# Kernel tuning notes

Measured on AMD Instinct MI355X. Metric: run time of the kernel, lower is better.

The kernel has to match this reference:

```python
import jax, jax.numpy as jnp
import numpy as np

MAX_PER_CLASS = 100   # max_num_boxes_per_class
MAX_TOTAL = 300       # max_num_boxes (pad_per_class=False -> output size is MAX_TOTAL)
IOU_THR = 0.5
SCORE_THR = 0.001
NEG = jnp.float32(-1e30)
EPS = 1e-12


def _canon(b):
    # boxes given as any diagonal pair (y1,x1,y2,x2); canonicalize like TF NMS
    ymin = jnp.minimum(b[..., 0], b[..., 2])
    ymax = jnp.maximum(b[..., 0], b[..., 2])
    xmin = jnp.minimum(b[..., 1], b[..., 3])
    xmax = jnp.maximum(b[..., 1], b[..., 3])
    return ymin, xmin, ymax, xmax


def _iou_one_vs_all(box, boxes):
    # box [4], boxes [N,4] -> iou [N]
    y1a, x1a, y2a, x2a = _canon(box)
    y1b, x1b, y2b, x2b = _canon(boxes)
    ih = jnp.maximum(jnp.minimum(y2a, y2b) - jnp.maximum(y1a, y1b), 0.0)
    iw = jnp.maximum(jnp.minimum(x2a, x2b) - jnp.maximum(x1a, x1b), 0.0)
    inter = ih * iw
    area_a = (y2a - y1a) * (x2a - x1a)
    area_b = (y2b - y1b) * (x2b - x1b)
    union = jnp.maximum(area_a + area_b - inter, EPS)
    return inter / union


def _nms_single_class(boxes_c, scores_c):
    # boxes_c [N,4], scores_c [N] -> (scores [K], boxes [K,4], valid [K]) with K=MAX_PER_CLASS
    N = scores_c.shape[0]
    valid = scores_c > SCORE_THR
    s = jnp.where(valid, scores_c, NEG)
    order = jnp.argsort(-s)
    b_sorted = boxes_c[order]          # [N,4]
    s_sorted = s[order]                # [N]
    v_sorted = valid[order]            # [N]

    def step(keep, xs):
        i, box_i, valid_i = xs
        iou_row = _iou_one_vs_all(box_i, b_sorted)          # [N]
        suppressed = jnp.any(keep & (iou_row > IOU_THR))    # vs previously kept only
        keep = keep.at[i].set(valid_i & jnp.logical_not(suppressed))
        return keep, None

    keep0 = jnp.zeros((N,), dtype=bool)
    keep, _ = jax.lax.scan(step, keep0, (jnp.arange(N), b_sorted, v_sorted))

    # cap number of kept boxes at MAX_PER_CLASS (in descending score order)
    rank = jnp.cumsum(keep.astype(jnp.int32)) - 1
    keep = keep & (rank < MAX_PER_CLASS)

    key = jnp.where(keep, s_sorted, NEG)
    top_s, top_i = jax.lax.top_k(key, MAX_PER_CLASS)
    top_boxes = b_sorted[top_i]
    top_valid = top_s > (NEG / 2)
    return top_s, top_boxes, top_valid


def _combined_nms(scores, boxes):
    # scores [B,N,C], boxes [B,N,q,4] with q==1 (boxes shared across classes)
    B, N, C = scores.shape
    q = boxes.shape[2]

    def per_image(scores_i, boxes_i):
        # scores_i [N,C], boxes_i [N,q,4]
        if q == 1:
            cls_boxes = jnp.broadcast_to(boxes_i, (N, C, 4))
        else:
            cls_boxes = boxes_i
        # per-class NMS, vmapped over the class axis
        sc, bx, vd = jax.vmap(_nms_single_class, in_axes=(1, 1))(cls_boxes, scores_i)
        # sc [C,K], bx [C,K,4], vd [C,K]
        cls_ids = jnp.broadcast_to(
            jnp.arange(C, dtype=scores.dtype)[:, None], vd.shape)

        flat_s = jnp.where(vd, sc, NEG).reshape(-1)   # [C*K]
        flat_b = bx.reshape(-1, 4)
        flat_c = cls_ids.reshape(-1)
        flat_v = vd.reshape(-1)

        top_s, idx = jax.lax.top_k(flat_s, MAX_TOTAL)
        out_v = flat_v[idx]
        out_s = jnp.where(out_v, top_s, 0.0)
        out_b = jnp.where(out_v[:, None], flat_b[idx], 0.0)
        out_b = jnp.clip(out_b, 0.0, 1.0)             # clip_boxes=True
        out_c = jnp.where(out_v, flat_c[idx], 0.0)
        count = jnp.sum(out_v.astype(jnp.int32))
        return out_s, out_b, out_c, count

    return jax.vmap(per_image)(scores, boxes)


def setup_inputs() -> dict:
    key = jax.random.key(0)
    k1, k2 = jax.random.split(key)
    B, N, C, Q = 4, 1024, 80, 1
    scores = jax.random.uniform(k1, (B, N, C), dtype=jnp.float32)
    boxes = jax.random.uniform(k2, (B, N, Q, 4), dtype=jnp.float32)
    return {"scores": scores, "boxes": boxes}


def reference(scores, boxes):
    # returns (output_scores, output_boxes, output_classes, valid_counts)
    return _combined_nms(scores, boxes)
```

## Files before the change

### kernel.cpp

```cpp
#include <hip/hip_runtime.h>
#include <stdint.h>

#define N_BOX 1024
#define C_CLS 80
#define B_IMG 4
#define K_PER 100
#define K_TOT 300
#define NEGF  (-1e30f)
#define NCAND (C_CLS * K_PER)
#define M_SEL 8192
#define KPAD  1088
#define EQCAP 768

#define OFF_DONE    0
#define OFF_WSCORE  1835008
#define OFF_WSIDX   1963008

typedef unsigned long long u64;
typedef unsigned int u32;

__device__ __forceinline__ int swz(int i) { return i + (i >> 4); }

__device__ __forceinline__ u32 ford(float f) {
    u32 u = __float_as_uint(f);
    return (u & 0x80000000u) ? ~u : (u | 0x80000000u);
}
__device__ __forceinline__ float funord(u32 o) {
    u32 u = (o & 0x80000000u) ? (o ^ 0x80000000u) : ~o;
    return __uint_as_float(u);
}

__device__ __forceinline__ bool iou_gt_fast(float4 a, float aa, float4 b, float ab) {
#pragma clang fp contract(off)
    float ih = fminf(a.z, b.z) - fmaxf(a.x, b.x); ih = fmaxf(ih, 0.0f);
    float iw = fminf(a.w, b.w) - fmaxf(a.y, b.y); iw = fmaxf(iw, 0.0f);
    float inter = ih * iw;
    float uni = fmaxf(aa + ab - inter, 1e-12f);
    float diff = 2.0f * inter - uni;
    bool kill = diff > uni * 2.4e-7f;
    if (__builtin_expect(!kill && diff > 0.0f, 0))
        kill = (inter / uni) > 0.5f;
    return kill;
}

__global__ __launch_bounds__(256, 2) void nms_classes(
        const float* __restrict__ scores,
        const float* __restrict__ boxes,
        float* __restrict__ ws_score,
        int*   __restrict__ ws_idx,
        float* __restrict__ out,
        int*   __restrict__ done_cnt)
{
    __shared__ u64    key[KPAD];
    __shared__ float4 bx[N_BOX];
    __shared__ float  ar[N_BOX];
    __shared__ float4 wbuf[2][64];
    __shared__ float  wab[2][64];
    __shared__ float4 kb[128];
    __shared__ float  ka[128];
    __shared__ int    kept_t[K_PER];
    __shared__ u32    colk16[4][64];
    __shared__ u64    sup64[4];
    __shared__ int    sh_nvalid, sh_kept, sh_rank;
    __shared__ u32    skey[NCAND];
    __shared__ u32    hist4[1024];
    __shared__ u64    list[512];
    __shared__ u32    eq[EQCAP];
    __shared__ int    sh_sel, sh_cnt, sh_valid, sh_eqcnt;
    __shared__ u32    sh_need;

    const int tid  = threadIdx.x;
    const int lane = tid & 63;
    const int b  = blockIdx.x / C_CLS;
    const int c  = blockIdx.x % C_CLS;

    if (tid == 0) { sh_nvalid = 0; sh_kept = 0; }

    for (int n = tid; n < N_BOX; n += 256) {
        float4 v = ((const float4*)boxes)[b * N_BOX + n];
        {
#pragma clang fp contract(off)
            float y1 = fminf(v.x, v.z), y2 = fmaxf(v.x, v.z);
            float x1 = fminf(v.y, v.w), x2 = fmaxf(v.y, v.w);
            bx[n] = make_float4(y1, x1, y2, x2);
            ar[n] = (y2 - y1) * (x2 - x1);
        }
    }
    __syncthreads();

    u64 r[4];
    {
        const float* sc = scores + (size_t)(b * N_BOX) * C_CLS + c;
        int lv = 0;
        #pragma unroll
        for (int q = 0; q < 4; ++q) {
            int v = tid * 4 + q;
            float s0 = sc[(size_t)v * C_CLS];
            bool valid = s0 > 0.001f;
            float s = valid ? s0 : NEGF;
            r[q] = ((u64)ford(s) << 32) | (u32)(N_BOX - 1 - v);
            lv += valid ? 1 : 0;
        }
        if (lv) atomicAdd(&sh_nvalid, lv);
    }

    #define CE(a, b, d) { u64 _mx = (a) > (b) ? (a) : (b); \
                          u64 _mn = (a) > (b) ? (b) : (a); \
                          (a) = (d) ? _mx : _mn; (b) = (d) ? _mn : _mx; }
    CE(r[0], r[1], true); CE(r[2], r[3], false);

    for (int k = 4; k <= N_BOX; k <<= 1) {
        const bool d = ((tid & (k >> 2)) == 0);
        for (int j = k >> 1; j > 0; j >>= 1) {
            if (j >= 256) {
                __syncthreads();
                #pragma unroll
                for (int q = 0; q < 4; ++q) key[swz(tid * 4 + q)] = r[q];
                __syncthreads();
                const bool upper = ((tid * 4) & j) != 0;
                #pragma unroll
                for (int q = 0; q < 4; ++q) {
                    u64 pv = key[swz((tid * 4 + q) ^ j)];
                    u64 mx = r[q] > pv ? r[q] : pv;
                    u64 mn = r[q] > pv ? pv : r[q];
                    r[q] = (d != upper) ? mx : mn;
                }
            } else if (j >= 4) {
                const int dl = j >> 2;
                const bool upper = (lane & dl) != 0;
                #pragma unroll
                for (int q = 0; q < 4; ++q) {
                    u64 pv = __shfl_xor(r[q], dl);
                    u64 mx = r[q] > pv ? r[q] : pv;
                    u64 mn = r[q] > pv ? pv : r[q];
                    r[q] = (d != upper) ? mx : mn;
                }
            } else if (j == 2) {
                CE(r[0], r[2], d); CE(r[1], r[3], d);
            } else {
                CE(r[0], r[1], d); CE(r[2], r[3], d);
            }
        }
    }
    #undef CE

    __syncthreads();
    #pragma unroll
    for (int q = 0; q < 4; ++q) key[swz(tid * 4 + q)] = r[q];
    __syncthreads();

    if (tid < 64) {
        u64 kv = key[swz(tid)];
        int idx = (N_BOX - 1) - (int)(u32)(kv & 0xFFFFFFFFu);
        wbuf[0][tid] = bx[idx];
        wab[0][tid]  = ar[idx];
    }

    const int nvalid = sh_nvalid;
    const int nwin = (nvalid + 63) >> 6;
    const int me  = tid & 63;
    const int grp = tid >> 6;

    for (int w = 0; w < nwin; ++w) {
        const int cur = w & 1;
        __syncthreads();
        if (sh_kept >= K_PER) break;
        const int kept0 = sh_kept;
        const int bt = w * 64;

        if (grp == 1 && (w + 1) < nwin) {
            u64 kv = key[swz((bt + 64 + me) & (N_BOX - 1))];
            int idx = (N_BOX - 1) - (int)(u32)(kv & 0xFFFFFFFFu);
            wbuf[cur ^ 1][me] = bx[idx];
            wab[cur ^ 1][me]  = ar[idx];
        }

        const float4 qm = wbuf[cur][me];
        const float  am = wab[cur][me];

        {
            float4 wrow[16]; float warow[16];
            #pragma unroll
            for (int rq = 0; rq < 16; ++rq) {
                wrow[rq]  = wbuf[cur][grp * 16 + rq];
                warow[rq] = wab[cur][grp * 16 + rq];
            }
            u32 bits = 0;
            #pragma unroll
            for (int rq = 0; rq < 16; ++rq) {
                int rr = grp * 16 + rq;
                bool kill = (rr != me) && iou_gt_fast(wrow[rq], warow[rq], qm, am);
                bits |= ((u32)kill) << rq;
            }
            colk16[grp][me] = bits;
        }

        {
            bool supme = false;
            for (int t0 = 0; grp + 4 * t0 < kept0; t0 += 8) {
                float4 kbl[8]; float kal[8];
                #pragma unroll
                for (int i = 0; i < 8; ++i) {
                    int k = grp + 4 * (t0 + i);
                    kbl[i] = kb[k]; kal[i] = ka[k];
                }
                #pragma unroll
                for (int i = 0; i < 8; ++i) {
                    int k = grp + 4 * (t0 + i);
                    if (k < kept0 && iou_gt_fast(kbl[i], kal[i], qm, am)) supme = true;
                }
            }
            u64 bal = __ballot(supme);
            if (lane == 0) sup64[grp] = bal;
        }
        __syncthreads();

        if (grp == 0) {
            u32 c0 = colk16[0][lane], c1 = colk16[1][lane];
            u32 c2 = colk16[2][lane], c3 = colk16[3][lane];
            u64 colkill = (u64)c0 | ((u64)c1 << 16)
                        | ((u64)c2 << 32) | ((u64)c3 << 48);
            u64 supp = sup64[0] | sup64[1] | sup64[2] | sup64[3];
            bool in = ((bt + lane) < nvalid) && !((supp >> lane) & 1ull);
            u64 pending = __ballot(in);
            int kept = kept0;
            u64 acc = 0;
            while (pending && kept < K_PER) {
                int t0 = __ffsll((long long)pending) - 1;
                acc |= 1ull << t0;
                kept++;
                bool kill = (colkill >> t0) & 1ull;
                pending &= ~(1ull << t0);
                pending &= ~__ballot(kill);
            }
            if ((acc >> lane) & 1ull) {
                int pos = kept0 + (int)__popcll(acc & ((1ull << lane) - 1ull));
                kept_t[pos] = bt + lane;
                kb[pos] = qm; ka[pos] = am;
            }
            if (lane == 0) sh_kept = kept;
        }
    }
    __syncthreads();

    const int kept = sh_kept;
    if (tid < K_PER) {
        int ob = (b * C_CLS + c) * K_PER + tid;
        if (tid < kept) {
            u64 k = key[swz(kept_t[tid])];
            ws_score[ob] = funord((u32)(k >> 32));
            ws_idx[ob]   = (N_BOX - 1) - (int)(u32)(k & 0xFFFFFFFFu);
        } else {
            ws_score[ob] = NEGF;
            ws_idx[ob]   = 0;
        }
    }

    __syncthreads();
    if (tid == 0) {
        __threadfence();
        sh_rank = atomicAdd(&done_cnt[b], 1);
    }
    __syncthreads();
    if (sh_rank != C_CLS - 1) return;
    __threadfence();

    const int base2 = b * NCAND;
    if (tid == 0) { sh_cnt = 0; sh_valid = 0; sh_eqcnt = 0; }
    for (int i = tid; i < NCAND / 4; i += 256) {
        float4 s4 = ((const float4*)(ws_score + base2))[i];
        skey[4 * i + 0] = ford(s4.x);
        skey[4 * i + 1] = ford(s4.y);
        skey[4 * i + 2] = ford(s4.z);
        skey[4 * i + 3] = ford(s4.w);
    }
    for (int i = tid; i < 512; i += 256) list[i] = 0;
    for (int i = tid; i < 1024; i += 256) hist4[i] = 0;
    __syncthreads();

    u64 prefix = 0;
    u32 need = K_TOT;
    const int rounds[6] = {7, 6, 5, 4, 1, 0};
    const int slot = tid & 3;

    for (int rd = 0; rd < 2; ++rd) {
        const int d = rounds[rd];
        for (int i0 = 0; i0 < NCAND; i0 += 1024) {
            u32 kv[4];
            #pragma unroll
            for (int q = 0; q < 4; ++q) {
                int i = i0 + tid + q * 256;
                kv[q] = (i < NCAND) ? skey[i] : 0u;
            }
            #pragma unroll
            for (int q = 0; q < 4; ++q) {
                int i = i0 + tid + q * 256;
                if (i < NCAND) {
                    u64 k = ((u64)kv[q] << 32) | (u32)(M_SEL - 1 - i);
                    bool match = (d == 7) || (((k ^ prefix) >> (8 * (d + 1))) == 0);
                    if (match)
                        atomicAdd(&hist4[(((u32)(k >> (8 * d)) & 0xFFu) << 2) | slot], 1u);
                }
            }
        }
        __syncthreads();
        if (tid < 64) {
            const int l = tid;
            u32 h[4];
            #pragma unroll
            for (int q = 0; q < 4; ++q) {
                int bin = 4 * l + q;
                h[q] = hist4[bin * 4 + 0] + hist4[bin * 4 + 1]
                     + hist4[bin * 4 + 2] + hist4[bin * 4 + 3];
                hist4[bin * 4 + 0] = 0; hist4[bin * 4 + 1] = 0;
                hist4[bin * 4 + 2] = 0; hist4[bin * 4 + 3] = 0;
            }
            u32 s3 = h[3], s2 = h[2] + s3, s1 = h[1] + s2, s0 = h[0] + s1;
            u32 tot = s0, S = tot;
            #pragma unroll
            for (int off = 1; off < 64; off <<= 1) {
                u32 t = __shfl(S, (l + off) & 63);
                if (l + off < 64) S += t;
            }
            u32 T = S - tot;
            u32 sv0 = s0 + T, sv1 = s1 + T, sv2 = s2 + T, sv3 = s3 + T;
            if (sv0 >= need && sv1 < need) { sh_sel = 4*l;     sh_need = need - sv1; }
            if (sv1 >= need && sv2 < need) { sh_sel = 4*l + 1; sh_need = need - sv2; }
            if (sv2 >= need && sv3 < need) { sh_sel = 4*l + 2; sh_need = need - sv3; }
            if (sv3 >= need && T   < need) { sh_sel = 4*l + 3; sh_need = need - T;   }
        }
        __syncthreads();
        prefix |= ((u64)(u32)sh_sel) << (8 * d);
        need = sh_need;
        __syncthreads();
    }

    {
        const u32 p16 = (u32)(prefix >> 48);
        for (int i0 = 0; i0 < NCAND; i0 += 1024) {
            u32 kv[4];
            #pragma unroll
            for (int q = 0; q < 4; ++q) {
                int i = i0 + tid + q * 256;
                kv[q] = (i < NCAND) ? skey[i] : 0u;
            }
            #pragma unroll
            for (int q = 0; q < 4; ++q) {
                int i = i0 + tid + q * 256;
                if (i < NCAND) {
                    u64 k = ((u64)kv[q] << 32) | (u32)(M_SEL - 1 - i);
                    u32 t16 = (u32)(k >> 48);
                    if (t16 > p16) {
                        int p = atomicAdd(&sh_cnt, 1);
                        if (p < 512) list[p] = k;
                    } else if (t16 == p16) {
                        int p = atomicAdd(&sh_eqcnt, 1);
                        if (p < EQCAP) eq[p] = (u32)i;
                    }
                }
            }
        }
    }
    __syncthreads();
    const int eqn_raw = sh_eqcnt;
    const bool over = eqn_raw > EQCAP;
    const int eqn = over ? 0 : eqn_raw;

    if (!over) {
        for (int rd = 2; rd < 6; ++rd) {
            const int d = rounds[rd];
            for (int j = tid; j < eqn; j += 256) {
                int i = eq[j];
                u64 k = ((u64)skey[i] << 32) | (u32)(M_SEL - 1 - i);
                bool match = (((k ^ prefix) >> (8 * (d + 1))) == 0);
                if (match)
                    atomicAdd(&hist4[(((u32)(k >> (8 * d)) & 0xFFu) << 2) | slot], 1u);
            }
            __syncthreads();
            if (tid < 64) {
                const int l = tid;
                u32 h[4];
                #pragma unroll
                for (int q = 0; q < 4; ++q) {
                    int bin = 4 * l + q;
                    h[q] = hist4[bin * 4 + 0] + hist4[bin * 4 + 1]
                         + hist4[bin * 4 + 2] + hist4[bin * 4 + 3];
                    hist4[bin * 4 + 0] = 0; hist4[bin * 4 + 1] = 0;
                    hist4[bin * 4 + 2] = 0; hist4[bin * 4 + 3] = 0;
                }
                u32 s3 = h[3], s2 = h[2] + s3, s1 = h[1] + s2, s0 = h[0] + s1;
                u32 tot = s0, S = tot;
                #pragma unroll
                for (int off = 1; off < 64; off <<= 1) {
                    u32 t = __shfl(S, (l + off) & 63);
                    if (l + off < 64) S += t;
                }
                u32 T = S - tot;
                u32 sv0 = s0 + T, sv1 = s1 + T, sv2 = s2 + T, sv3 = s3 + T;
                if (sv0 >= need && sv1 < need) { sh_sel = 4*l;     sh_need = need - sv1; }
                if (sv1 >= need && sv2 < need) { sh_sel = 4*l + 1; sh_need = need - sv2; }
                if (sv2 >= need && sv3 < need) { sh_sel = 4*l + 2; sh_need = need - sv3; }
                if (sv3 >= need && T   < need) { sh_sel = 4*l + 3; sh_need = need - T;   }
            }
            __syncthreads();
            prefix |= ((u64)(u32)sh_sel) << (8 * d);
            need = sh_need;
            __syncthreads();
        }

        for (int j = tid; j < eqn; j += 256) {
            int i = eq[j];
            u64 k = ((u64)skey[i] << 32) | (u32)(M_SEL - 1 - i);
            if (k >= prefix) {
                int p = atomicAdd(&sh_cnt, 1);
                if (p < 512) list[p] = k;
            }
        }
    } else {
        __syncthreads();
        for (int i = tid; i < 512; i += 256) list[i] = 0;
        if (tid == 0) sh_cnt = 0;
        __syncthreads();
        for (int rd = 2; rd < 6; ++rd) {
            const int d = rounds[rd];
            for (int i0 = 0; i0 < NCAND; i0 += 1024) {
                u32 kv[4];
                #pragma unroll
                for (int q = 0; q < 4; ++q) {
                    int i = i0 + tid + q * 256;
                    kv[q] = (i < NCAND) ? skey[i] : 0u;
                }
                #pragma unroll
                for (int q = 0; q < 4; ++q) {
                    int i = i0 + tid + q * 256;
                    if (i < NCAND) {
                        u64 k = ((u64)kv[q] << 32) | (u32)(M_SEL - 1 - i);
                        bool match = (((k ^ prefix) >> (8 * (d + 1))) == 0);
                        if (match)
                            atomicAdd(&hist4[(((u32)(k >> (8 * d)) & 0xFFu) << 2) | slot], 1u);
                    }
                }
            }
            __syncthreads();
            if (tid < 64) {
                const int l = tid;
                u32 h[4];
                #pragma unroll
                for (int q = 0; q < 4; ++q) {
                    int bin = 4 * l + q;
                    h[q] = hist4[bin * 4 + 0] + hist4[bin * 4 + 1]
                         + hist4[bin * 4 + 2] + hist4[bin * 4 + 3];
                    hist4[bin * 4 + 0] = 0; hist4[bin * 4 + 1] = 0;
                    hist4[bin * 4 + 2] = 0; hist4[bin * 4 + 3] = 0;
                }
                u32 s3 = h[3], s2 = h[2] + s3, s1 = h[1] + s2, s0 = h[0] + s1;
                u32 tot = s0, S = tot;
                #pragma unroll
                for (int off = 1; off < 64; off <<= 1) {
                    u32 t = __shfl(S, (l + off) & 63);
                    if (l + off < 64) S += t;
                }
                u32 T = S - tot;
                u32 sv0 = s0 + T, sv1 = s1 + T, sv2 = s2 + T, sv3 = s3 + T;
                if (sv0 >= need && sv1 < need) { sh_sel = 4*l;     sh_need = need - sv1; }
                if (sv1 >= need && sv2 < need) { sh_sel = 4*l + 1; sh_need = need - sv2; }
                if (sv2 >= need && sv3 < need) { sh_sel = 4*l + 2; sh_need = need - sv3; }
                if (sv3 >= need && T   < need) { sh_sel = 4*l + 3; sh_need = need - T;   }
            }
            __syncthreads();
            prefix |= ((u64)(u32)sh_sel) << (8 * d);
            need = sh_need;
            __syncthreads();
        }
        for (int i0 = 0; i0 < NCAND; i0 += 1024) {
            u32 kv[4];
            #pragma unroll
            for (int q = 0; q < 4; ++q) {
                int i = i0 + tid + q * 256;
                kv[q] = (i < NCAND) ? skey[i] : 0u;
            }
            #pragma unroll
            for (int q = 0; q < 4; ++q) {
                int i = i0 + tid + q * 256;
                if (i < NCAND) {
                    u64 k = ((u64)kv[q] << 32) | (u32)(M_SEL - 1 - i);
                    if (k >= prefix) {
                        int p = atomicAdd(&sh_cnt, 1);
                        if (p < 512) list[p] = k;
                    }
                }
            }
        }
    }
    __syncthreads();

    if (tid < 64) {
        const int l = tid;
        u64 e[8];
        #pragma unroll
        for (int q = 0; q < 8; ++q) e[q] = list[l * 8 + q];
        #define CE2(a, b, dd) { u64 _mx = (a) > (b) ? (a) : (b); \
                                u64 _mn = (a) > (b) ? (b) : (a); \
                                (a) = (dd) ? _mx : _mn; (b) = (dd) ? _mn : _mx; }
        CE2(e[0], e[1], true);  CE2(e[2], e[3], false);
        CE2(e[4], e[5], true);  CE2(e[6], e[7], false);
        CE2(e[0], e[2], true);  CE2(e[1], e[3], true);
        CE2(e[4], e[6], false); CE2(e[5], e[7], false);
        CE2(e[0], e[1], true);  CE2(e[2], e[3], true);
        CE2(e[4], e[5], false); CE2(e[6], e[7], false);
        for (int k = 8; k <= 512; k <<= 1) {
            const bool d = ((l & (k >> 3)) == 0);
            for (int j = k >> 1; j >= 8; j >>= 1) {
                const int dl = j >> 3;
                const bool upper = (l & dl) != 0;
                #pragma unroll
                for (int q = 0; q < 8; ++q) {
                    u64 pv = __shfl_xor(e[q], dl);
                    u64 mx = e[q] > pv ? e[q] : pv;
                    u64 mn = e[q] > pv ? pv : e[q];
                    e[q] = (d != upper) ? mx : mn;
                }
            }
            CE2(e[0], e[4], d); CE2(e[1], e[5], d);
            CE2(e[2], e[6], d); CE2(e[3], e[7], d);
            CE2(e[0], e[2], d); CE2(e[1], e[3], d);
            CE2(e[4], e[6], d); CE2(e[5], e[7], d);
            CE2(e[0], e[1], d); CE2(e[2], e[3], d);
            CE2(e[4], e[5], d); CE2(e[6], e[7], d);
        }
        #undef CE2
        #pragma unroll
        for (int q = 0; q < 8; ++q) list[l * 8 + q] = e[q];
    }
    __syncthreads();

    float* out_s = out;
    float* out_b = out + B_IMG * K_TOT;
    float* out_c = out + B_IMG * K_TOT * 5;
    float* out_n = out + B_IMG * K_TOT * 6;

    for (int i = tid; i < K_TOT; i += 256) {
        u64 k = list[i];
        float s = funord((u32)(k >> 32));
        int flat = (M_SEL - 1) - (int)(u32)(k & 0xFFFFFFFFu);
        bool valid = s > (-5e29f);
        float os = 0.0f, oc = 0.0f;
        float4 obv = make_float4(0.0f, 0.0f, 0.0f, 0.0f);
        if (valid && flat < NCAND) {
            int cc = flat / K_PER;
            int n  = ws_idx[base2 + flat];
            float4 bb = ((const float4*)boxes)[b * N_BOX + n];
            os = s;
            oc = (float)cc;
            obv.x = fminf(fmaxf(bb.x, 0.0f), 1.0f);
            obv.y = fminf(fmaxf(bb.y, 0.0f), 1.0f);
            obv.z = fminf(fmaxf(bb.z, 0.0f), 1.0f);
            obv.w = fminf(fmaxf(bb.w, 0.0f), 1.0f);
            atomicAdd(&sh_valid, 1);
        }
        out_s[b * K_TOT + i] = os;
        ((float4*)out_b)[b * K_TOT + i] = obv;
        out_c[b * K_TOT + i] = oc;
    }
    __syncthreads();
    if (tid == 0) out_n[b] = (float)sh_valid;
}

extern "C" void kernel_launch(void* const* d_in, const int* in_sizes, int n_in,
                              void* d_out, int out_size, void* d_ws, size_t ws_size,
                              hipStream_t stream) {
    const float* scores = (const float*)d_in[0];
    const float* boxes  = (const float*)d_in[1];

    char* ws = (char*)d_ws;
    int*   done_cnt = (int*)(ws + OFF_DONE);
    float* ws_score = (float*)(ws + OFF_WSCORE);
    int*   ws_idx   = (int*)  (ws + OFF_WSIDX);

    hipMemsetAsync(done_cnt, 0, B_IMG * sizeof(int), stream);
    nms_classes<<<dim3(B_IMG * C_CLS), dim3(256), 0, stream>>>(
        scores, boxes, ws_score, ws_idx, (float*)d_out, done_cnt);
}
```

Measured before the change: 120.1 us.

## Split final cross-class top-k into separate 1024-thread kernel

Removes the last-block-done pattern (memset of counters, threadfence, atomic rank) from the per-class NMS kernel and moves the per-image top-300 radix select into a second kernel launched with one 1024-thread block per image. This drops the large merge-stage shared arrays from the NMS kernel, shrinking its LDS footprint, and lets the final select run with four times as many threads. In exchange it adds a kernel launch boundary and a global round-trip of the workspace between kernels.

```diff
diff --git a/kernel.cpp b/kernel.cpp
--- a/kernel.cpp
+++ b/kernel.cpp
@@ -12,7 +12,6 @@
 #define KPAD  1088
 #define EQCAP 768
 
-#define OFF_DONE    0
 #define OFF_WSCORE  1835008
 #define OFF_WSIDX   1963008
 
@@ -47,9 +46,7 @@
         const float* __restrict__ scores,
         const float* __restrict__ boxes,
         float* __restrict__ ws_score,
-        int*   __restrict__ ws_idx,
-        float* __restrict__ out,
-        int*   __restrict__ done_cnt)
+        int*   __restrict__ ws_idx)
 {
     __shared__ u64    key[KPAD];
     __shared__ float4 bx[N_BOX];
@@ -61,13 +58,7 @@
     __shared__ int    kept_t[K_PER];
     __shared__ u32    colk16[4][64];
     __shared__ u64    sup64[4];
-    __shared__ int    sh_nvalid, sh_kept, sh_rank;
-    __shared__ u32    skey[NCAND];
-    __shared__ u32    hist4[1024];
-    __shared__ u64    list[512];
-    __shared__ u32    eq[EQCAP];
-    __shared__ int    sh_sel, sh_cnt, sh_valid, sh_eqcnt;
-    __shared__ u32    sh_need;
+    __shared__ int    sh_nvalid, sh_kept;
 
     const int tid  = threadIdx.x;
     const int lane = tid & 63;
@@ -255,27 +246,35 @@
             ws_idx[ob]   = 0;
         }
     }
-
-    __syncthreads();
-    if (tid == 0) {
-        __threadfence();
-        sh_rank = atomicAdd(&done_cnt[b], 1);
-    }
-    __syncthreads();
-    if (sh_rank != C_CLS - 1) return;
-    __threadfence();
-
-    const int base2 = b * NCAND;
+}
+
+__global__ __launch_bounds__(1024) void final_topk(
+        const float* __restrict__ ws_score,
+        const int*   __restrict__ ws_idx,
+        const float* __restrict__ boxes,
+        float* __restrict__ out)
+{
+    __shared__ u32 skey[NCAND];
+    __shared__ u32 hist4[1024];
+    __shared__ u64 list[512];
+    __shared__ u32 eq[EQCAP];
+    __shared__ int sh_sel, sh_cnt, sh_valid, sh_eqcnt;
+    __shared__ u32 sh_need;
+
+    const int tid = threadIdx.x;
+    const int b = blockIdx.x;
+    const int base = b * NCAND;
+
     if (tid == 0) { sh_cnt = 0; sh_valid = 0; sh_eqcnt = 0; }
-    for (int i = tid; i < NCAND / 4; i += 256) {
-        float4 s4 = ((const float4*)(ws_score + base2))[i];
+    for (int i = tid; i < NCAND / 4; i += 1024) {
+        float4 s4 = ((const float4*)(ws_score + base))[i];
         skey[4 * i + 0] = ford(s4.x);
         skey[4 * i + 1] = ford(s4.y);
         skey[4 * i + 2] = ford(s4.z);
         skey[4 * i + 3] = ford(s4.w);
     }
-    for (int i = tid; i < 512; i += 256) list[i] = 0;
-    for (int i = tid; i < 1024; i += 256) hist4[i] = 0;
+    if (tid < 512) list[tid] = 0;
+    hist4[tid] = 0;
     __syncthreads();
 
     u64 prefix = 0;
@@ -285,16 +284,16 @@
 
     for (int rd = 0; rd < 2; ++rd) {
         const int d = rounds[rd];
-        for (int i0 = 0; i0 < NCAND; i0 += 1024) {
+        for (int i0 = 0; i0 < NCAND; i0 += 4096) {
             u32 kv[4];
             #pragma unroll
             for (int q = 0; q < 4; ++q) {
-                int i = i0 + tid + q * 256;
+                int i = i0 + tid + q * 1024;
                 kv[q] = (i < NCAND) ? skey[i] : 0u;
             }
             #pragma unroll
             for (int q = 0; q < 4; ++q) {
-                int i = i0 + tid + q * 256;
+                int i = i0 + tid + q * 1024;
                 if (i < NCAND) {
                     u64 k = ((u64)kv[q] << 32) | (u32)(M_SEL - 1 - i);
                     bool match = (d == 7) || (((k ^ prefix) >> (8 * (d + 1))) == 0);
@@ -337,20 +336,20 @@
 
     {
         const u32 p16 = (u32)(prefix >> 48);
-        for (int i0 = 0; i0 < NCAND; i0 += 1024) {
+        for (int i0 = 0; i0 < NCAND; i0 += 4096) {
             u32 kv[4];
             #pragma unroll
             for (int q = 0; q < 4; ++q) {
-                int i = i0 + tid + q * 256;
+                int i = i0 + tid + q * 1024;
                 kv[q] = (i < NCAND) ? skey[i] : 0u;
             }
             #pragma unroll
             for (int q = 0; q < 4; ++q) {
-                int i = i0 + tid + q * 256;
+                int i = i0 + tid + q * 1024;
                 if (i < NCAND) {
                     u64 k = ((u64)kv[q] << 32) | (u32)(M_SEL - 1 - i);
                     u32 t16 = (u32)(k >> 48);
-                    if (t16 > p16) {
+                    if (t16 > (u32)(prefix >> 48)) {
                         int p = atomicAdd(&sh_cnt, 1);
                         if (p < 512) list[p] = k;
                     } else if (t16 == p16) {
@@ -369,7 +368,7 @@
     if (!over) {
         for (int rd = 2; rd < 6; ++rd) {
             const int d = rounds[rd];
-            for (int j = tid; j < eqn; j += 256) {
+            for (int j = tid; j < eqn; j += 1024) {
                 int i = eq[j];
                 u64 k = ((u64)skey[i] << 32) | (u32)(M_SEL - 1 - i);
                 bool match = (((k ^ prefix) >> (8 * (d + 1))) == 0);
@@ -408,7 +407,7 @@
             __syncthreads();
         }
 
-        for (int j = tid; j < eqn; j += 256) {
+        for (int j = tid; j < eqn; j += 1024) {
             int i = eq[j];
             u64 k = ((u64)skey[i] << 32) | (u32)(M_SEL - 1 - i);
             if (k >= prefix) {
@@ -418,21 +417,21 @@
         }
     } else {
         __syncthreads();
-        for (int i = tid; i < 512; i += 256) list[i] = 0;
+        if (tid < 512) list[tid] = 0;
         if (tid == 0) sh_cnt = 0;
         __syncthreads();
         for (int rd = 2; rd < 6; ++rd) {
             const int d = rounds[rd];
-            for (int i0 = 0; i0 < NCAND; i0 += 1024) {
+            for (int i0 = 0; i0 < NCAND; i0 += 4096) {
                 u32 kv[4];
                 #pragma unroll
                 for (int q = 0; q < 4; ++q) {
-                    int i = i0 + tid + q * 256;
+                    int i = i0 + tid + q * 1024;
                     kv[q] = (i < NCAND) ? skey[i] : 0u;
                 }
                 #pragma unroll
                 for (int q = 0; q < 4; ++q) {
-                    int i = i0 + tid + q * 256;
+                    int i = i0 + tid + q * 1024;
                     if (i < NCAND) {
                         u64 k = ((u64)kv[q] << 32) | (u32)(M_SEL - 1 - i);
                         bool match = (((k ^ prefix) >> (8 * (d + 1))) == 0);
@@ -472,16 +471,16 @@
             need = sh_need;
             __syncthreads();
         }
-        for (int i0 = 0; i0 < NCAND; i0 += 1024) {
+        for (int i0 = 0; i0 < NCAND; i0 += 4096) {
             u32 kv[4];
             #pragma unroll
             for (int q = 0; q < 4; ++q) {
-                int i = i0 + tid + q * 256;
+                int i = i0 + tid + q * 1024;
                 kv[q] = (i < NCAND) ? skey[i] : 0u;
             }
             #pragma unroll
             for (int q = 0; q < 4; ++q) {
-                int i = i0 + tid + q * 256;
+                int i = i0 + tid + q * 1024;
                 if (i < NCAND) {
                     u64 k = ((u64)kv[q] << 32) | (u32)(M_SEL - 1 - i);
                     if (k >= prefix) {
@@ -539,7 +538,7 @@
     float* out_c = out + B_IMG * K_TOT * 5;
     float* out_n = out + B_IMG * K_TOT * 6;
 
-    for (int i = tid; i < K_TOT; i += 256) {
+    for (int i = tid; i < K_TOT; i += 1024) {
         u64 k = list[i];
         float s = funord((u32)(k >> 32));
         int flat = (M_SEL - 1) - (int)(u32)(k & 0xFFFFFFFFu);
@@ -548,7 +547,7 @@
         float4 obv = make_float4(0.0f, 0.0f, 0.0f, 0.0f);
         if (valid && flat < NCAND) {
             int cc = flat / K_PER;
-            int n  = ws_idx[base2 + flat];
+            int n  = ws_idx[base + flat];
             float4 bb = ((const float4*)boxes)[b * N_BOX + n];
             os = s;
             oc = (float)cc;
@@ -573,11 +572,11 @@
     const float* boxes  = (const float*)d_in[1];
 
     char* ws = (char*)d_ws;
-    int*   done_cnt = (int*)(ws + OFF_DONE);
     float* ws_score = (float*)(ws + OFF_WSCORE);
     int*   ws_idx   = (int*)  (ws + OFF_WSIDX);
 
-    hipMemsetAsync(done_cnt, 0, B_IMG * sizeof(int), stream);
     nms_classes<<<dim3(B_IMG * C_CLS), dim3(256), 0, stream>>>(
-        scores, boxes, ws_score, ws_idx, (float*)d_out, done_cnt);
+        scores, boxes, ws_score, ws_idx);
+    final_topk<<<dim3(B_IMG), dim3(1024), 0, stream>>>(
+        ws_score, ws_idx, boxes, (float*)d_out);
 }
```

Measured after the change: 110.6 us. -7.9%, faster.
